# Optimization experiments

Hardware: AMD Instinct MI355X
Metric: run time of the kernel (lower is better)

## Reference

```python
import jax, jax.numpy as jnp
import numpy as np

B, H, W = 16, 128, 128
R = 4          # reward_dim
A = 8          # action_channels
K = 3          # receptive_field
P = K // 2     # padding
I = R + 1      # reward_and_value_dim
PAD_VALUE = 0.0


def setup_inputs() -> dict:
    key = jax.random.key(0)
    k1, k2, k3 = jax.random.split(key, 3)
    values = jax.random.normal(k1, (B, H, W), dtype=jnp.float32)
    rewards = jax.random.normal(k2, (B, R, H, W), dtype=jnp.float32)
    # conv weight: out = A * I * K * K channels, in = I, kernel KxK (no bias)
    fan_in = I * K * K
    weight = jax.random.normal(k3, (A * I * K * K, I, K, K), dtype=jnp.float32) / np.sqrt(fan_in)
    return {"values": values, "rewards": rewards, "weight": weight}


def reference(values, rewards, weight):
    b, h, w = values.shape
    # pack([rewards, values], 'b * h w') -> [b, I, h, w]
    rv = jnp.concatenate([rewards, values[:, None]], axis=1)
    padded = jnp.pad(rv, ((0, 0), (0, 0), (P, P), (P, P)), constant_values=PAD_VALUE)
    # dynamic per-pixel transition kernels: conv2d -> [b, A*I*K*K, h, w]
    dyn = jax.lax.conv_general_dilated(
        padded, weight, window_strides=(1, 1), padding='VALID',
        dimension_numbers=('NCHW', 'OIHW', 'NCHW'))
    # rearrange 'b (o i k1 k2) h w -> b o (i k1 k2) h w' (o outermost in channel dim)
    dyn = dyn.reshape(b, A, I * K * K, h, w)
    dyn = jax.nn.softmax(dyn, axis=2)
    # unfold: patches [b, I*K*K, h, w], channel-major then (k1, k2) row-major (matches F.unfold)
    patches = jnp.stack(
        [padded[:, :, di:di + h, dj:dj + w] for di in range(K) for dj in range(K)],
        axis=2)  # [b, I, K*K, h, w]
    patches = patches.reshape(b, I * K * K, h, w)
    # q_values: per-pixel weighted sum over the I*K*K neighborhood features
    q_values = jnp.einsum('bihw,boihw->bohw', patches, dyn)
    # max-pool over actions (logsumexp_pool=False)
    next_values = jnp.max(q_values, axis=1)
    return next_values
```

## Files before the change

kernel.cpp:

```cpp
#include <hip/hip_runtime.h>
#include <math.h>

#define BB 16
#define HH 128
#define WW 128
#define RR 4
#define AA 8
#define II 5
#define CC 45
#define NPIX (BB*HH*WW)
#define LOG2E 1.4426950408889634f

typedef __attribute__((ext_vector_type(8))) short v8s;
typedef __attribute__((ext_vector_type(4))) float v4f;
typedef __attribute__((ext_vector_type(4))) unsigned short v4u16;

__device__ __align__(16) unsigned short g_wbf[AA * 3072];

__device__ __forceinline__ unsigned short f2bf(float f) {
    union { float f; unsigned int u; } v; v.f = f;
    unsigned int r = v.u + 0x7fffu + ((v.u >> 16) & 1u);
    return (unsigned short)(r >> 16);
}

__global__ __launch_bounds__(256) void repack_kernel(const float* __restrict__ w) {
    const int e = blockIdx.x * 256 + threadIdx.x;
    if (e >= AA * 3072) return;
    const int o    = e / 3072;
    const int rem  = e - o * 3072;
    const int mtks = rem >> 9;
    const int l    = (rem >> 3) & 63;
    const int j    = rem & 7;
    const int mt   = mtks >> 1;
    const int ks   = mtks & 1;
    const int ch   = mt * 16 + (l & 15);
    const int k    = ks * 32 + (l >> 4) * 8 + j;
    float v = 0.0f;
    if (ch < CC && k < CC) v = w[(o * CC + ch) * CC + k] * LOG2E;
    g_wbf[e] = f2bf(v);
}

__global__ __launch_bounds__(128, 4) void vi_mfma(
    const float* __restrict__ values,
    const float* __restrict__ rewards,
    float* __restrict__ out)
{
    __shared__ __align__(16) unsigned short lds[2 * 64 * 72];
    const int lane = threadIdx.x & 63;
    const int wv   = threadIdx.x >> 6;
    const int c    = lane & 15;
    const int g    = lane >> 4;
    const int row  = blockIdx.x;
    const int b    = row >> 7;
    const int h    = row & 127;
    const int w0   = wv * 64;
    const int P0   = row * 128 + w0;
    const int wbase = wv * (64 * 72);

    {
        v8s z = {0,0,0,0,0,0,0,0};
        #pragma unroll
        for (int qq = 0; qq < 9; ++qq)
            *(v8s*)(&lds[wbase + lane * 72 + qq * 8]) = z;
    }

    #pragma unroll
    for (int t = 0; t < 4; ++t) {
        const int pw = w0 + t * 16 + c;
        #pragma unroll
        for (int tt = 0; tt < 12; ++tt) {
            const int j = g * 12 + tt;
            if (j < CC) {
                const int i  = j / 9;
                const int r9 = j - i * 9;
                const int k1 = r9 / 3;
                const int k2 = r9 - k1 * 3;
                const int y = h + k1 - 1;
                const int x = pw + k2 - 1;
                float f = 0.0f;
                if (y >= 0 && y < HH && x >= 0 && x < WW)
                    f = (i < RR) ? rewards[((b * RR + i) * HH + y) * WW + x]
                                 : values[(b * HH + y) * WW + x];
                lds[wbase + (t * 16 + c) * 72 + j] = f2bf(f);
            }
        }
    }

    v8s Bf[4][2];
    #pragma unroll
    for (int t = 0; t < 4; ++t)
        #pragma unroll
        for (int ks = 0; ks < 2; ++ks)
            Bf[t][ks] = *(const v8s*)(&lds[wbase + (t * 16 + c) * 72 + ks * 32 + g * 8]);

    v4u16 pu[4][3];
    #pragma unroll
    for (int t = 0; t < 4; ++t)
        #pragma unroll
        for (int mt = 0; mt < 3; ++mt)
            pu[t][mt] = *(const v4u16*)(&lds[wbase + (t * 16 + c) * 72 + mt * 16 + g * 4]);

    float best[4] = {-1e30f, -1e30f, -1e30f, -1e30f};
    const unsigned short* wb = g_wbf;

    #pragma unroll 1
    for (int o = 0; o < AA; ++o) {
        v8s Af[3][2];
        #pragma unroll
        for (int mt = 0; mt < 3; ++mt)
            #pragma unroll
            for (int ks = 0; ks < 2; ++ks)
                Af[mt][ks] = *(const v8s*)(wb + (o * 6 + mt * 2 + ks) * 512 + lane * 8);
        #pragma unroll
        for (int t = 0; t < 4; ++t) {
            v4f acc[3];
            #pragma unroll
            for (int mt = 0; mt < 3; ++mt) {
                acc[mt] = (v4f){0.f, 0.f, 0.f, 0.f};
                acc[mt] = __builtin_amdgcn_mfma_f32_16x16x32_bf16(Af[mt][0], Bf[t][0], acc[mt], 0, 0, 0);
                acc[mt] = __builtin_amdgcn_mfma_f32_16x16x32_bf16(Af[mt][1], Bf[t][1], acc[mt], 0, 0, 0);
            }
            float s = 0.f, q = 0.f;
            #pragma unroll
            for (int mt = 0; mt < 3; ++mt) {
                #pragma unroll
                for (int r = 0; r < 4; ++r) {
                    const float e  = __builtin_amdgcn_exp2f(acc[mt][r]);
                    const float pv = __uint_as_float(((unsigned int)pu[t][mt][r]) << 16);
                    s += e;
                    q = fmaf(e, pv, q);
                }
            }
            s += __shfl_xor(s, 16);  q += __shfl_xor(q, 16);
            s += __shfl_xor(s, 32);  q += __shfl_xor(q, 32);
            best[t] = fmaxf(best[t], q * __builtin_amdgcn_rcpf(s - 3.0f));
        }
    }

    if (g == 0) {
        #pragma unroll
        for (int t = 0; t < 4; ++t)
            out[P0 + t * 16 + c] = best[t];
    }
}

extern "C" void kernel_launch(void* const* d_in, const int* in_sizes, int n_in,
                              void* d_out, int out_size, void* d_ws, size_t ws_size,
                              hipStream_t stream) {
    const float* values  = (const float*)d_in[0];
    const float* rewards = (const float*)d_in[1];
    const float* weight  = (const float*)d_in[2];
    float* out = (float*)d_out;

    repack_kernel<<<96, 256, 0, stream>>>(weight);
    vi_mfma<<<2048, 128, 0, stream>>>(values, rewards, out);
}
```

Measured before the change: 93.31 us.

## Halve pixels per wave, double grid, shrink LDS row stride

Each wave now handles 32 pixels instead of 64, and the grid doubles to 4096 blocks. The LDS row stride drops from 72 to 56, and the second K-slice B fragment is zero-filled in registers for lanes past the valid channels. Launch bounds rise to 6 blocks per SM. The aim is higher occupancy and fewer registers and less LDS per wave, to hide load latency better. The cost is that each A-fragment weight load per action is now amortised over half as many pixels.

```diff
diff --git a/kernel.cpp b/kernel.cpp
--- a/kernel.cpp
+++ b/kernel.cpp
@@ -10,6 +10,7 @@
 #define CC 45
 #define NPIX (BB*HH*WW)
 #define LOG2E 1.4426950408889634f
+#define RS 56
 
 typedef __attribute__((ext_vector_type(8))) short v8s;
 typedef __attribute__((ext_vector_type(4))) float v4f;
@@ -40,32 +41,33 @@
     g_wbf[e] = f2bf(v);
 }
 
-__global__ __launch_bounds__(128, 4) void vi_mfma(
+__global__ __launch_bounds__(128, 6) void vi_mfma(
     const float* __restrict__ values,
     const float* __restrict__ rewards,
     float* __restrict__ out)
 {
-    __shared__ __align__(16) unsigned short lds[2 * 64 * 72];
+    __shared__ __align__(16) unsigned short lds[2 * 32 * RS];
     const int lane = threadIdx.x & 63;
     const int wv   = threadIdx.x >> 6;
     const int c    = lane & 15;
     const int g    = lane >> 4;
-    const int row  = blockIdx.x;
-    const int b    = row >> 7;
-    const int h    = row & 127;
-    const int w0   = wv * 64;
-    const int P0   = row * 128 + w0;
-    const int wbase = wv * (64 * 72);
+    const int P0   = (blockIdx.x * 2 + wv) * 32;
+    const int b    = P0 >> 14;
+    const int h    = (P0 >> 7) & 127;
+    const int w0   = P0 & 127;
+    const int wbase = wv * (32 * RS);
 
     {
         v8s z = {0,0,0,0,0,0,0,0};
         #pragma unroll
-        for (int qq = 0; qq < 9; ++qq)
-            *(v8s*)(&lds[wbase + lane * 72 + qq * 8]) = z;
+        for (int qq = 0; qq < 4; ++qq) {
+            const int slot = qq * 64 + lane;
+            if (slot < 224) *(v8s*)(&lds[wbase + slot * 8]) = z;
+        }
     }
 
     #pragma unroll
-    for (int t = 0; t < 4; ++t) {
+    for (int t = 0; t < 2; ++t) {
         const int pw = w0 + t * 16 + c;
         #pragma unroll
         for (int tt = 0; tt < 12; ++tt) {
@@ -81,26 +83,29 @@
                 if (y >= 0 && y < HH && x >= 0 && x < WW)
                     f = (i < RR) ? rewards[((b * RR + i) * HH + y) * WW + x]
                                  : values[(b * HH + y) * WW + x];
-                lds[wbase + (t * 16 + c) * 72 + j] = f2bf(f);
+                lds[wbase + (t * 16 + c) * RS + j] = f2bf(f);
             }
         }
     }
 
-    v8s Bf[4][2];
+    v8s Bf[2][2];
     #pragma unroll
-    for (int t = 0; t < 4; ++t)
-        #pragma unroll
-        for (int ks = 0; ks < 2; ++ks)
-            Bf[t][ks] = *(const v8s*)(&lds[wbase + (t * 16 + c) * 72 + ks * 32 + g * 8]);
+    for (int t = 0; t < 2; ++t) {
+        const int rbase = wbase + (t * 16 + c) * RS;
+        Bf[t][0] = *(const v8s*)(&lds[rbase + g * 8]);
+        if (g < 2) Bf[t][1] = *(const v8s*)(&lds[rbase + 32 + g * 8]);
+        else       Bf[t][1] = (v8s){0,0,0,0,0,0,0,0};
+    }
 
-    v4u16 pu[4][3];
+    v4u16 pu[2][3];
     #pragma unroll
-    for (int t = 0; t < 4; ++t)
+    for (int t = 0; t < 2; ++t)
         #pragma unroll
         for (int mt = 0; mt < 3; ++mt)
-            pu[t][mt] = *(const v4u16*)(&lds[wbase + (t * 16 + c) * 72 + mt * 16 + g * 4]);
+            pu[t][mt] = *(const v4u16*)(&lds[wbase + (t * 16 + c) * RS
+                                             + mt * 16 + g * 4]);
 
-    float best[4] = {-1e30f, -1e30f, -1e30f, -1e30f};
+    float best[2] = {-1e30f, -1e30f};
     const unsigned short* wb = g_wbf;
 
     #pragma unroll 1
@@ -112,7 +117,7 @@
             for (int ks = 0; ks < 2; ++ks)
                 Af[mt][ks] = *(const v8s*)(wb + (o * 6 + mt * 2 + ks) * 512 + lane * 8);
         #pragma unroll
-        for (int t = 0; t < 4; ++t) {
+        for (int t = 0; t < 2; ++t) {
             v4f acc[3];
             #pragma unroll
             for (int mt = 0; mt < 3; ++mt) {
@@ -139,7 +144,7 @@
 
     if (g == 0) {
         #pragma unroll
-        for (int t = 0; t < 4; ++t)
+        for (int t = 0; t < 2; ++t)
             out[P0 + t * 16 + c] = best[t];
     }
 }
@@ -153,5 +158,5 @@
     float* out = (float*)d_out;
 
     repack_kernel<<<96, 256, 0, stream>>>(weight);
-    vi_mfma<<<2048, 128, 0, stream>>>(values, rewards, out);
+    vi_mfma<<<4096, 128, 0, stream>>>(values, rewards, out);
 }
```

After: 99.16 us. +6.3%, slower.
